# Performance work log

Measured on AMD Instinct MI355X. Metric: run time of the kernel, lower is better.

The kernel has to match this reference:

```python
import jax, jax.numpy as jnp
import numpy as np
from jax import lax

EMB = 30
K = 5

def leaky(x):
    return jnp.where(x > 0, x, 0.1 * x)

def conv_resid(x, W, b):
    # x: [L, EMB]; W: [EMB, EMB, 3]; SAME trigram conv (matches torch pad=2 + slice) + residual
    y = lax.conv_general_dilated(x.T[None], W, window_strides=(1,), padding=[(1, 1)])  # [1,EMB,L]
    y = leaky(y + b[None, :, None])
    return y[0].T + x

def cosine_sim(A, B):
    num = A @ B.T                                   # [Qa, Qb]
    den = jnp.linalg.norm(A, axis=1)[:, None] * jnp.linalg.norm(B, axis=1)[None, :]
    return num / den

def kmax_pool(sim):
    top = lax.top_k(sim, K)[0]                      # [Q, K] descending
    return jnp.stack([top[:, 0], top.mean(axis=-1)], axis=-1)  # [Q, 2]

def get_output(pools, w, W1, W2):
    temp = jnp.concatenate(pools, axis=-1)          # [Q, 6]
    lo = leaky(temp @ W1.T) @ W2.T                  # [Q, 1]
    lo = lo[:, 0] * w
    return lo.sum() / lo.shape[0]

def setup_inputs() -> dict:
    key = jax.random.key(0)
    ks = jax.random.split(key, 12)
    Q, D = 2048, 8192
    inp = {
        "doc1_embeds": jax.random.normal(ks[0], (D, EMB), jnp.float32),
        "doc2_embeds": jax.random.normal(ks[1], (D, EMB), jnp.float32),
        "question_embeds": jax.random.normal(ks[2], (Q, EMB), jnp.float32),
        "q_idfs": jax.random.uniform(ks[3], (Q, 1), jnp.float32),
        "gaf": jax.random.uniform(ks[4], (4,), jnp.float32),
        "baf": jax.random.uniform(ks[5], (4,), jnp.float32),
        "W_conv": jax.random.normal(ks[6], (EMB, EMB, 3), jnp.float32) * 0.1,
        "b_conv": jax.random.normal(ks[7], (EMB,), jnp.float32) * 0.1,
        "W_qw": jax.random.normal(ks[8], (1, EMB + 1), jnp.float32) * 0.1,
        "W_q1": jax.random.normal(ks[9], (8, 6), jnp.float32) * 0.3,
        "W_q2": jax.random.normal(ks[10], (1, 8), jnp.float32) * 0.3,
        "W_out": jax.random.normal(ks[11], (1, 5), jnp.float32) * 0.3,
    }
    return inp

def reference(doc1_embeds, doc2_embeds, question_embeds, q_idfs, gaf, baf,
              W_conv, b_conv, W_qw, W_q1, W_q2, W_out):
    sim_i_d1 = cosine_sim(question_embeds, doc1_embeds)
    sim_i_d2 = cosine_sim(question_embeds, doc2_embeds)
    sim_oh_d1 = (sim_i_d1 > 1 - 0.001).astype(jnp.float32)
    sim_oh_d2 = (sim_i_d2 > 1 - 0.001).astype(jnp.float32)
    q_conv = conv_resid(question_embeds, W_conv, b_conv)
    d1_conv = conv_resid(doc1_embeds, W_conv, b_conv)
    d2_conv = conv_resid(doc2_embeds, W_conv, b_conv)
    sim_s_d1 = cosine_sim(q_conv, d1_conv)
    sim_s_d2 = cosine_sim(q_conv, d2_conv)
    q_weights = jax.nn.softmax((jnp.concatenate([q_conv, q_idfs], axis=-1) @ W_qw.T)[:, 0])
    doc1_emit = get_output([kmax_pool(sim_oh_d1), kmax_pool(sim_i_d1), kmax_pool(sim_s_d1)], q_weights, W_q1, W_q2)
    doc2_emit = get_output([kmax_pool(sim_oh_d2), kmax_pool(sim_i_d2), kmax_pool(sim_s_d2)], q_weights, W_q1, W_q2)
    good_out = jnp.concatenate([gaf, doc1_emit[None]]) @ W_out.T  # [1]
    bad_out = jnp.concatenate([baf, doc2_emit[None]]) @ W_out.T   # [1]
    loss1 = jnp.sum(jax.nn.relu(1.0 + bad_out - good_out), axis=-1)
    return (loss1, good_out, bad_out)
```

## Files before the change

### kernel.cpp

```cpp
#include <hip/hip_runtime.h>
#include <hip/hip_bf16.h>
#include <math.h>

#define EMB 30
#define NS 32
#define JT 256
#define SUB 64

typedef __attribute__((ext_vector_type(8))) short bf16x8;
typedef __attribute__((ext_vector_type(4))) float f32x4;
typedef __attribute__((ext_vector_type(4))) unsigned u32x4;
typedef __attribute__((ext_vector_type(2))) _Float16 f16x2;

__device__ __forceinline__ float leakyf(float x) { return x > 0.0f ? x : 0.1f * x; }

__device__ __forceinline__ unsigned short f2b(float x) {
  __hip_bfloat16 h = __float2bfloat16(x);
  union { __hip_bfloat16 h; unsigned short u; } cv;
  cv.h = h;
  return cv.u;
}

__device__ __forceinline__ unsigned pkmax(unsigned a, unsigned b) {
  unsigned d;
  asm("v_pk_max_f16 %0, %1, %2" : "=v"(d) : "v"(a), "v"(b));
  return d;
}
__device__ __forceinline__ unsigned pkmin(unsigned a, unsigned b) {
  unsigned d;
  asm("v_pk_min_f16 %0, %1, %2" : "=v"(d) : "v"(a), "v"(b));
  return d;
}
__device__ __forceinline__ unsigned cvtpku(float a, float b) {
  return __builtin_bit_cast(unsigned, __builtin_amdgcn_cvt_pkrtz(a, b));
}

__device__ __forceinline__ void ins5h(unsigned (&t)[5], unsigned v) {
  unsigned n0 = pkmax(t[0], v);
  unsigned n1 = pkmax(pkmin(t[0], v), t[1]);
  unsigned n2 = pkmax(pkmin(t[1], v), t[2]);
  unsigned n3 = pkmax(pkmin(t[2], v), t[3]);
  unsigned n4 = pkmax(pkmin(t[3], v), t[4]);
  t[0] = n0; t[1] = n1; t[2] = n2; t[3] = n3; t[4] = n4;
}

__device__ __forceinline__ void merge5h(unsigned (&a)[5], const unsigned (&b)[5]) {
  unsigned c0 = pkmax(a[0], b[0]);
  unsigned c1 = pkmax(pkmax(pkmin(a[0], b[0]), a[1]), b[1]);
  unsigned c2 = pkmax(pkmax(pkmin(a[0], b[1]), pkmin(a[1], b[0])), pkmax(a[2], b[2]));
  unsigned c3 = pkmax(pkmax(pkmin(a[0], b[2]), pkmin(a[1], b[1])),
                      pkmax(pkmin(a[2], b[0]), pkmax(a[3], b[3])));
  unsigned c4 = pkmax(pkmax(pkmax(pkmin(a[0], b[3]), pkmin(a[1], b[2])),
                            pkmax(pkmin(a[2], b[1]), pkmin(a[3], b[0]))),
                      pkmax(a[4], b[4]));
  a[0] = c0; a[1] = c1; a[2] = c2; a[3] = c3; a[4] = c4;
}

__device__ __forceinline__ void merge5(float (&a)[5], const float (&b)[5]) {
  float c0 = fmaxf(a[0], b[0]);
  float c1 = fmaxf(fmaxf(fminf(a[0], b[0]), a[1]), b[1]);
  float c2 = fmaxf(fmaxf(fminf(a[0], b[1]), fminf(a[1], b[0])), fmaxf(a[2], b[2]));
  float c3 = fmaxf(fmaxf(fminf(a[0], b[2]), fminf(a[1], b[1])),
                   fmaxf(fminf(a[2], b[0]), fmaxf(a[3], b[3])));
  float c4 = fmaxf(fmaxf(fmaxf(fminf(a[0], b[3]), fminf(a[1], b[2])),
                         fmaxf(fminf(a[2], b[1]), fminf(a[3], b[0]))),
                   fmaxf(a[4], b[4]));
  a[0] = c0; a[1] = c1; a[2] = c2; a[3] = c3; a[4] = c4;
}

template <int PAT>
__device__ __forceinline__ void bfly_round(unsigned (&t)[8][5]) {
#pragma unroll
  for (int li = 0; li < 8; ++li) {
    unsigned b[5];
#pragma unroll
    for (int k = 0; k < 5; ++k)
      b[k] = (unsigned)__builtin_amdgcn_ds_swizzle((int)t[li][k], PAT);
    merge5h(t[li], b);
  }
}

__global__ __launch_bounds__(256) void prep_all_kernel(
    const float* __restrict__ Xq, const float* __restrict__ X1,
    const float* __restrict__ X2, int Q, int D,
    const float* __restrict__ Wc, const float* __restrict__ bc,
    const float* __restrict__ qidf, const float* __restrict__ Wqw,
    unsigned short* __restrict__ qr, unsigned short* __restrict__ qc,
    unsigned short* __restrict__ cmb, float* __restrict__ logits) {
  __shared__ float sX[258 * EMB];
  int tid = threadIdx.x;
  int nbQ = Q >> 8, nbD = D >> 8;
  int b = blockIdx.x;
  const float* X;
  int L, l0, slot = 0;
  bool isQ = false;
  if (b < nbQ) { X = Xq; L = Q; l0 = b << 8; isQ = true; }
  else if (b < nbQ + nbD) { X = X1; L = D; l0 = (b - nbQ) << 8; slot = 0; }
  else { X = X2; L = D; l0 = (b - nbQ - nbD) << 8; slot = 2; }

  int base = l0 * EMB - EMB;
  int lim = L * EMB;
  for (int idx = tid; idx < 258 * EMB; idx += 256) {
    int g = base + idx;
    sX[idx] = (g >= 0 && g < lim) ? X[g] : 0.0f;
  }
  __syncthreads();

  int l = l0 + tid;
  float xm[EMB], x0[EMB], xp[EMB], y[EMB];
#pragma unroll
  for (int i = 0; i < EMB; ++i) xm[i] = sX[tid * EMB + i];
#pragma unroll
  for (int i = 0; i < EMB; ++i) x0[i] = sX[(tid + 1) * EMB + i];
#pragma unroll
  for (int i = 0; i < EMB; ++i) xp[i] = sX[(tid + 2) * EMB + i];

  float sr = 0.0f, sc = 0.0f, lg = 0.0f;
#pragma unroll
  for (int i = 0; i < EMB; ++i) sr += x0[i] * x0[i];
#pragma unroll 1
  for (int o = 0; o < EMB; ++o) {
    float acc = bc[o];
#pragma unroll
    for (int i = 0; i < EMB; ++i) {
      acc += Wc[o * 90 + i * 3 + 0] * xm[i];
      acc += Wc[o * 90 + i * 3 + 1] * x0[i];
      acc += Wc[o * 90 + i * 3 + 2] * xp[i];
    }
    float v = leakyf(acc) + x0[o];
    y[o] = v;
    sc += v * v;
    lg += v * Wqw[o];
  }
  float rnr = 1.0f / sqrtf(sr);
  float rnc = 1.0f / sqrtf(sc);
  if (isQ) logits[l] = lg + qidf[l] * Wqw[EMB];

  unsigned int rp[16], cp[16];
#pragma unroll
  for (int k = 0; k < 15; ++k) {
    rp[k] = (unsigned int)f2b(x0[2 * k] * rnr) | ((unsigned int)f2b(x0[2 * k + 1] * rnr) << 16);
    cp[k] = (unsigned int)f2b(y[2 * k] * rnc) | ((unsigned int)f2b(y[2 * k + 1] * rnc) << 16);
  }
  rp[15] = 0u; cp[15] = 0u;
  if (isQ) {
    unsigned int* rw = (unsigned int*)(qr + (size_t)l * 32);
    unsigned int* cw = (unsigned int*)(qc + (size_t)l * 32);
#pragma unroll
    for (int k = 0; k < 16; ++k) { rw[k] = rp[k]; cw[k] = cp[k]; }
  } else {
    unsigned int* rowp = (unsigned int*)(cmb + (size_t)l * 128);
    int sx = (l & 7) << 2;
#pragma unroll
    for (int k = 0; k < 16; ++k) {
      rowp[(slot * 16 + k) ^ sx]       = rp[k];
      rowp[((slot + 1) * 16 + k) ^ sx] = cp[k];
    }
  }
}

__global__ __launch_bounds__(256) void main_kernel(
    const unsigned short* __restrict__ qrA, const unsigned short* __restrict__ qcA,
    const unsigned* __restrict__ cmb32,
    float* __restrict__ partials, int Q, int D) {
  __shared__ __align__(16) unsigned lds[2][SUB * 64];
  int tid = threadIdx.x;
  int wave = tid >> 6, lane = tid & 63;
  int lo = lane & 15, hi = lane >> 4;
  int qt = blockIdx.x >> 5, ds = blockIdx.x & (NS - 1);
  int qrow = qt * 64 + wave * 16 + lo;
  bf16x8 aR = *(const bf16x8*)(qrA + (size_t)qrow * 32 + hi * 8);
  bf16x8 aC = *(const bf16x8*)(qcA + (size_t)qrow * 32 + hi * 8);

  unsigned t[8][5];
#pragma unroll
  for (int li = 0; li < 8; ++li)
#pragma unroll
    for (int k = 0; k < 5; ++k) t[li][k] = 0xC000C000u;

  const u32x4* gsrc = (const u32x4*)(cmb32 + (size_t)ds * JT * 64);
  u32x4 R[4];
#pragma unroll
  for (int i = 0; i < 4; ++i) R[i] = gsrc[i * 256 + tid];
#pragma unroll
  for (int i = 0; i < 4; ++i) ((u32x4*)lds[0])[i * 256 + tid] = R[i];

  int swzA = ((lo & 7) << 2);
  int c0 = (0  + hi * 4) ^ swzA;
  int c1 = (16 + hi * 4) ^ swzA;
  int c2 = (32 + hi * 4) ^ swzA;
  int c3 = (48 + hi * 4) ^ swzA;

#pragma unroll 1
  for (int st = 0; st < 4; ++st) {
    __syncthreads();
    if (st < 3) {
#pragma unroll
      for (int i = 0; i < 4; ++i) R[i] = gsrc[(st + 1) * 1024 + i * 256 + tid];
    }
    const unsigned* L = lds[st & 1];
#pragma unroll
    for (int it = 0; it < 4; ++it) {
      const unsigned* rp = L + (it * 16 + lo) * 64;
      bf16x8 X0 = *(const bf16x8*)(rp + c0);
      bf16x8 X1 = *(const bf16x8*)(rp + c1);
      bf16x8 X2 = *(const bf16x8*)(rp + c2);
      bf16x8 X3 = *(const bf16x8*)(rp + c3);
      f32x4 z = {0.0f, 0.0f, 0.0f, 0.0f};
      f32x4 s0 = __builtin_amdgcn_mfma_f32_16x16x32_bf16(aR, X0, z, 0, 0, 0);
      f32x4 s1 = __builtin_amdgcn_mfma_f32_16x16x32_bf16(aC, X1, z, 0, 0, 0);
      f32x4 s2 = __builtin_amdgcn_mfma_f32_16x16x32_bf16(aR, X2, z, 0, 0, 0);
      f32x4 s3 = __builtin_amdgcn_mfma_f32_16x16x32_bf16(aC, X3, z, 0, 0, 0);
#pragma unroll
      for (int r = 0; r < 4; ++r) {
        ins5h(t[r * 2 + 0], cvtpku(s0[r], s2[r]));
        ins5h(t[r * 2 + 1], cvtpku(s1[r], s3[r]));
      }
    }
    __syncthreads();
    if (st < 3) {
#pragma unroll
      for (int i = 0; i < 4; ++i) ((u32x4*)lds[(st + 1) & 1])[i * 256 + tid] = R[i];
    }
  }

  bfly_round<0x041F>(t);
  bfly_round<0x081F>(t);
  bfly_round<0x101F>(t);
  bfly_round<0x201F>(t);

  if (lo == 0) {
#pragma unroll
    for (int r = 0; r < 4; ++r) {
      int q = qt * 64 + wave * 16 + hi * 4 + r;
      float* dst = partials + ((size_t)q * NS + ds) * 20;
#pragma unroll
      for (int k = 0; k < 5; ++k) {
        f16x2 t0 = __builtin_bit_cast(f16x2, t[r * 2 + 0][k]);
        f16x2 t1 = __builtin_bit_cast(f16x2, t[r * 2 + 1][k]);
        dst[k]      = (float)t0[0];
        dst[5 + k]  = (float)t1[0];
        dst[10 + k] = (float)t0[1];
        dst[15 + k] = (float)t1[1];
      }
    }
  }
}

__global__ __launch_bounds__(256) void pool_kernel(
    const float* __restrict__ logits, const float* __restrict__ partials,
    const float* __restrict__ W1, const float* __restrict__ W2,
    float* __restrict__ blockSums, int Q) {
  __shared__ float sred[4];
  __shared__ float sP[8 * 641];
  int tid = threadIdx.x;
  int lane = tid & 63, wave = tid >> 6;

  float lmax = -3.0e38f;
  for (int q = tid; q < Q; q += 256) lmax = fmaxf(lmax, logits[q]);
#pragma unroll
  for (int m = 1; m < 64; m <<= 1) lmax = fmaxf(lmax, __shfl_xor(lmax, m));
  if (lane == 0) sred[wave] = lmax;
  __syncthreads();
  float M = fmaxf(fmaxf(sred[0], sred[1]), fmaxf(sred[2], sred[3]));
  __syncthreads();
  float lsum = 0.0f;
  for (int q = tid; q < Q; q += 256) lsum += expf(logits[q] - M);
#pragma unroll
  for (int m = 1; m < 64; m <<= 1) lsum += __shfl_xor(lsum, m);
  if (lane == 0) sred[wave] = lsum;
  __syncthreads();
  float rS = 1.0f / (sred[0] + sred[1] + sred[2] + sred[3]);

  size_t base = (size_t)blockIdx.x * 8 * NS * 20;
  for (int k = tid; k < 8 * NS * 20; k += 256) {
    int ql = k / 640, r = k - ql * 640;
    sP[ql * 641 + r] = partials[base + k];
  }
  __syncthreads();

  int ql = tid >> 5, dsp = tid & 31;
  int qglob = blockIdx.x * 8 + ql;
  float T[4][5];
#pragma unroll
  for (int li = 0; li < 4; ++li)
#pragma unroll
    for (int k = 0; k < 5; ++k) T[li][k] = sP[ql * 641 + dsp * 20 + li * 5 + k];
#pragma unroll
  for (int m = 16; m >= 1; m >>= 1) {
#pragma unroll
    for (int li = 0; li < 4; ++li) {
      float b[5];
#pragma unroll
      for (int k = 0; k < 5; ++k) b[k] = __shfl_xor(T[li][k], m);
      merge5(T[li], b);
    }
  }
  float s1 = 0.0f, s2 = 0.0f;
  if (dsp == 0) {
    float w = expf(logits[qglob] - M) * rS;
#pragma unroll
    for (int d = 0; d < 2; ++d) {
      const float (&Ti)[5] = T[d ? 2 : 0];
      const float (&Ts)[5] = T[d ? 3 : 1];
      float c = 0.0f;
#pragma unroll
      for (int k = 0; k < 5; ++k) c += (Ti[k] > 0.999f) ? 1.0f : 0.0f;
      float tmp[6];
      tmp[0] = (Ti[0] > 0.999f) ? 1.0f : 0.0f;
      tmp[1] = c * 0.2f;
      tmp[2] = Ti[0];
      tmp[3] = (Ti[0] + Ti[1] + Ti[2] + Ti[3] + Ti[4]) * 0.2f;
      tmp[4] = Ts[0];
      tmp[5] = (Ts[0] + Ts[1] + Ts[2] + Ts[3] + Ts[4]) * 0.2f;
      float lov = 0.0f;
#pragma unroll
      for (int r = 0; r < 8; ++r) {
        float h = 0.0f;
#pragma unroll
        for (int cidx = 0; cidx < 6; ++cidx) h += W1[r * 6 + cidx] * tmp[cidx];
        lov += W2[r] * leakyf(h);
      }
      if (d == 0) s1 = lov * w; else s2 = lov * w;
    }
  }
  __shared__ float r1[4], r2[4];
#pragma unroll
  for (int m = 1; m < 64; m <<= 1) { s1 += __shfl_xor(s1, m); s2 += __shfl_xor(s2, m); }
  if (lane == 0) { r1[wave] = s1; r2[wave] = s2; }
  __syncthreads();
  if (tid == 0) {
    blockSums[blockIdx.x * 2]     = r1[0] + r1[1] + r1[2] + r1[3];
    blockSums[blockIdx.x * 2 + 1] = r2[0] + r2[1] + r2[2] + r2[3];
  }
}

__global__ __launch_bounds__(64) void final_kernel(
    const float* __restrict__ blockSums, int nBlocks,
    const float* __restrict__ gaf, const float* __restrict__ baf,
    const float* __restrict__ Wout, float* __restrict__ out, int Q) {
  int tid = threadIdx.x;
  float s1 = 0.0f, s2 = 0.0f;
  for (int b = tid; b < nBlocks; b += 64) {
    s1 += blockSums[b * 2];
    s2 += blockSums[b * 2 + 1];
  }
#pragma unroll
  for (int m = 1; m < 64; m <<= 1) { s1 += __shfl_xor(s1, m); s2 += __shfl_xor(s2, m); }
  if (tid == 0) {
    float e1 = s1 / (float)Q, e2 = s2 / (float)Q;
    float good = gaf[0] * Wout[0] + gaf[1] * Wout[1] + gaf[2] * Wout[2] + gaf[3] * Wout[3] + e1 * Wout[4];
    float bad  = baf[0] * Wout[0] + baf[1] * Wout[1] + baf[2] * Wout[2] + baf[3] * Wout[3] + e2 * Wout[4];
    float loss = fmaxf(0.0f, 1.0f + bad - good);
    out[0] = loss; out[1] = good; out[2] = bad;
  }
}

extern "C" void kernel_launch(void* const* d_in, const int* in_sizes, int n_in,
                              void* d_out, int out_size, void* d_ws, size_t ws_size,
                              hipStream_t stream) {
  const float* d1   = (const float*)d_in[0];
  const float* d2   = (const float*)d_in[1];
  const float* qe   = (const float*)d_in[2];
  const float* qidf = (const float*)d_in[3];
  const float* gaf  = (const float*)d_in[4];
  const float* baf  = (const float*)d_in[5];
  const float* Wc   = (const float*)d_in[6];
  const float* bc   = (const float*)d_in[7];
  const float* Wqw  = (const float*)d_in[8];
  const float* Wq1  = (const float*)d_in[9];
  const float* Wq2  = (const float*)d_in[10];
  const float* Wout = (const float*)d_in[11];
  int D = in_sizes[0] / EMB;
  int Q = in_sizes[2] / EMB;

  unsigned short* us = (unsigned short*)d_ws;
  unsigned short* cmb = us; us += (size_t)D * 128;
  unsigned short* qrA = us; us += (size_t)Q * 32;
  unsigned short* qcA = us; us += (size_t)Q * 32;
  float* fp = (float*)us;
  float* logits    = fp; fp += Q;
  float* partials  = fp; fp += (size_t)Q * NS * 20;
  float* blockSums = fp; fp += (Q / 8) * 2;

  int grid = (Q >> 8) + 2 * (D >> 8);
  prep_all_kernel<<<grid, 256, 0, stream>>>(qe, d1, d2, Q, D, Wc, bc, qidf, Wqw,
                                            qrA, qcA, cmb, logits);
  main_kernel<<<(Q / 64) * NS, 256, 0, stream>>>(qrA, qcA, (const unsigned*)cmb,
                                                 partials, Q, D);
  pool_kernel<<<Q / 8, 256, 0, stream>>>(logits, partials, Wq1, Wq2, blockSums, Q);
  final_kernel<<<1, 64, 0, stream>>>(blockSums, Q / 8, gaf, baf, Wout, (float*)d_out, Q);
}
```

Measured before the change: 65.31 us.

## Split prep conv across four threads per row and stage weights in LDS

The prep kernel now handles 64 rows per block with four threads per row, each computing eight of the output channels. Squared norms and logits are combined with lane shuffles. Conv weights, bias and query weights are staged in shared memory instead of read from global memory in the inner loop. The goal is more blocks and less serial work per thread, since the old grid launched few blocks. In exchange there is some redundant weight loading per block and extra shuffle reductions.

Measured after the change: 57.41 us. 12.1% less time.

```diff
diff --git a/kernel.cpp b/kernel.cpp
--- a/kernel.cpp
+++ b/kernel.cpp
@@ -87,74 +87,96 @@
     const float* __restrict__ qidf, const float* __restrict__ Wqw,
     unsigned short* __restrict__ qr, unsigned short* __restrict__ qc,
     unsigned short* __restrict__ cmb, float* __restrict__ logits) {
-  __shared__ float sX[258 * EMB];
+  __shared__ float sX[66 * EMB];
+  __shared__ float sW[EMB * EMB * 3];
+  __shared__ float sB[EMB];
+  __shared__ float sQw[EMB + 1];
   int tid = threadIdx.x;
-  int nbQ = Q >> 8, nbD = D >> 8;
+  int nbQ = Q >> 6, nbD = D >> 6;
   int b = blockIdx.x;
   const float* X;
   int L, l0, slot = 0;
   bool isQ = false;
-  if (b < nbQ) { X = Xq; L = Q; l0 = b << 8; isQ = true; }
-  else if (b < nbQ + nbD) { X = X1; L = D; l0 = (b - nbQ) << 8; slot = 0; }
-  else { X = X2; L = D; l0 = (b - nbQ - nbD) << 8; slot = 2; }
-
+  if (b < nbQ) { X = Xq; L = Q; l0 = b << 6; isQ = true; }
+  else if (b < nbQ + nbD) { X = X1; L = D; l0 = (b - nbQ) << 6; slot = 0; }
+  else { X = X2; L = D; l0 = (b - nbQ - nbD) << 6; slot = 2; }
+
+  for (int idx = tid; idx < EMB * EMB * 3; idx += 256) sW[idx] = Wc[idx];
+  if (tid < EMB) sB[tid] = bc[tid];
+  if (tid < EMB + 1) sQw[tid] = Wqw[tid];
   int base = l0 * EMB - EMB;
   int lim = L * EMB;
-  for (int idx = tid; idx < 258 * EMB; idx += 256) {
+  for (int idx = tid; idx < 66 * EMB; idx += 256) {
     int g = base + idx;
     sX[idx] = (g >= 0 && g < lim) ? X[g] : 0.0f;
   }
   __syncthreads();
 
-  int l = l0 + tid;
-  float xm[EMB], x0[EMB], xp[EMB], y[EMB];
-#pragma unroll
-  for (int i = 0; i < EMB; ++i) xm[i] = sX[tid * EMB + i];
-#pragma unroll
-  for (int i = 0; i < EMB; ++i) x0[i] = sX[(tid + 1) * EMB + i];
-#pragma unroll
-  for (int i = 0; i < EMB; ++i) xp[i] = sX[(tid + 2) * EMB + i];
-
-  float sr = 0.0f, sc = 0.0f, lg = 0.0f;
-#pragma unroll
-  for (int i = 0; i < EMB; ++i) sr += x0[i] * x0[i];
-#pragma unroll 1
-  for (int o = 0; o < EMB; ++o) {
-    float acc = bc[o];
-#pragma unroll
-    for (int i = 0; i < EMB; ++i) {
-      acc += Wc[o * 90 + i * 3 + 0] * xm[i];
-      acc += Wc[o * 90 + i * 3 + 1] * x0[i];
-      acc += Wc[o * 90 + i * 3 + 2] * xp[i];
-    }
-    float v = leakyf(acc) + x0[o];
-    y[o] = v;
-    sc += v * v;
-    lg += v * Wqw[o];
-  }
+  int r = tid >> 2, sub = tid & 3;
+  int l = l0 + r;
+  int o0 = sub * 8;
+  const float* xmP = sX + r * EMB;
+  const float* x0P = sX + (r + 1) * EMB;
+  const float* xpP = sX + (r + 2) * EMB;
+  const float* wP  = sW + o0 * 90;
+
+  float acc[8];
+#pragma unroll
+  for (int oo = 0; oo < 8; ++oo)
+    acc[oo] = (o0 + oo < EMB) ? sB[o0 + oo] : 0.0f;
+  float sr = 0.0f;
+  for (int i = 0; i < EMB; ++i) {
+    float xm = xmP[i], x0v = x0P[i], xp = xpP[i];
+    sr += x0v * x0v;
+#pragma unroll
+    for (int oo = 0; oo < 8; ++oo) {
+      if (o0 + oo < EMB) {
+        acc[oo] += wP[oo * 90 + i * 3 + 0] * xm;
+        acc[oo] += wP[oo * 90 + i * 3 + 1] * x0v;
+        acc[oo] += wP[oo * 90 + i * 3 + 2] * xp;
+      }
+    }
+  }
+  float y[8];
+  float sc = 0.0f, lg = 0.0f;
+#pragma unroll
+  for (int oo = 0; oo < 8; ++oo) {
+    if (o0 + oo < EMB) {
+      float v = leakyf(acc[oo]) + x0P[o0 + oo];
+      y[oo] = v;
+      sc += v * v;
+      lg += v * sQw[o0 + oo];
+    } else y[oo] = 0.0f;
+  }
+  sc += __shfl_xor(sc, 1); sc += __shfl_xor(sc, 2);
+  lg += __shfl_xor(lg, 1); lg += __shfl_xor(lg, 2);
   float rnr = 1.0f / sqrtf(sr);
   float rnc = 1.0f / sqrtf(sc);
-  if (isQ) logits[l] = lg + qidf[l] * Wqw[EMB];
-
-  unsigned int rp[16], cp[16];
-#pragma unroll
-  for (int k = 0; k < 15; ++k) {
-    rp[k] = (unsigned int)f2b(x0[2 * k] * rnr) | ((unsigned int)f2b(x0[2 * k + 1] * rnr) << 16);
-    cp[k] = (unsigned int)f2b(y[2 * k] * rnc) | ((unsigned int)f2b(y[2 * k + 1] * rnc) << 16);
-  }
-  rp[15] = 0u; cp[15] = 0u;
+  if (isQ && sub == 0) logits[l] = lg + qidf[l] * sQw[EMB];
+
+  unsigned rd[4], cd[4];
+#pragma unroll
+  for (int kk = 0; kk < 4; ++kk) {
+    int k = sub * 4 + kk;
+    if (k < 15) {
+      rd[kk] = (unsigned)f2b(x0P[2 * k] * rnr) | ((unsigned)f2b(x0P[2 * k + 1] * rnr) << 16);
+      int oo = 2 * k - o0;
+      cd[kk] = (unsigned)f2b(y[oo] * rnc) | ((unsigned)f2b(y[oo + 1] * rnc) << 16);
+    } else { rd[kk] = 0u; cd[kk] = 0u; }
+  }
   if (isQ) {
-    unsigned int* rw = (unsigned int*)(qr + (size_t)l * 32);
-    unsigned int* cw = (unsigned int*)(qc + (size_t)l * 32);
-#pragma unroll
-    for (int k = 0; k < 16; ++k) { rw[k] = rp[k]; cw[k] = cp[k]; }
+    unsigned* rw = (unsigned*)(qr + (size_t)l * 32);
+    unsigned* cw = (unsigned*)(qc + (size_t)l * 32);
+#pragma unroll
+    for (int kk = 0; kk < 4; ++kk) { rw[sub * 4 + kk] = rd[kk]; cw[sub * 4 + kk] = cd[kk]; }
   } else {
-    unsigned int* rowp = (unsigned int*)(cmb + (size_t)l * 128);
+    unsigned* rowp = (unsigned*)(cmb + (size_t)l * 128);
     int sx = (l & 7) << 2;
 #pragma unroll
-    for (int k = 0; k < 16; ++k) {
-      rowp[(slot * 16 + k) ^ sx]       = rp[k];
-      rowp[((slot + 1) * 16 + k) ^ sx] = cp[k];
+    for (int kk = 0; kk < 4; ++kk) {
+      int k = sub * 4 + kk;
+      rowp[(slot * 16 + k) ^ sx]       = rd[kk];
+      rowp[((slot + 1) * 16 + k) ^ sx] = cd[kk];
     }
   }
 }
@@ -383,7 +405,7 @@
   float* partials  = fp; fp += (size_t)Q * NS * 20;
   float* blockSums = fp; fp += (Q / 8) * 2;
 
-  int grid = (Q >> 8) + 2 * (D >> 8);
+  int grid = (Q >> 6) + 2 * (D >> 6);
   prep_all_kernel<<<grid, 256, 0, stream>>>(qe, d1, d2, Q, D, Wc, bc, qidf, Wqw,
                                             qrA, qcA, cmb, logits);
   main_kernel<<<(Q / 64) * NS, 256, 0, stream>>>(qrA, qcA, (const unsigned*)cmb,
```
